# Kernel optimization log

Measured on AMD Instinct MI355X. Metric: run time of the kernel, lower is better.

## Reference

```python
import jax, jax.numpy as jnp
import numpy as np

TAU = 0.25
N_TIMESTEPS = 12


def setup_inputs() -> dict:
    key = jax.random.key(0)
    ks = jax.random.split(key, 6)
    B, O, H, P, C = 2048, 512, 1024, 1024, 512
    sc = lambda k, shape: jax.random.normal(k, shape, dtype=jnp.float32) * (1.0 / np.sqrt(shape[0]))
    return {
        "inputs": jax.random.normal(ks[0], (B, O), dtype=jnp.float32),
        "w_oh": sc(ks[1], (O, H)),
        "w_hp": sc(ks[2], (H, P)),
        "w_pp": sc(ks[3], (P, P)),
        "w_pc": sc(ks[4], (P, C)),
        "w_cp": sc(ks[5], (C, P)),
        "bias_h": jnp.zeros((H,), dtype=jnp.float32),
        "bias_p": jnp.zeros((P,), dtype=jnp.float32),
        "bias_c": jnp.zeros((C,), dtype=jnp.float32),
    }


def reference(inputs, w_oh, w_hp, w_pp, w_pc, w_cp, bias_h, bias_p, bias_c):
    tau = jnp.float32(TAU)
    one_m_tau = jnp.float32(1.0 - TAU)
    act = jax.nn.sigmoid
    B = inputs.shape[0]
    H, P, C = w_oh.shape[1], w_pp.shape[0], w_pc.shape[1]

    # tf.linalg.set_diag(w_pp, zeros) -> zero the self-connections
    w_pp0 = w_pp * (1.0 - jnp.eye(P, dtype=w_pp.dtype))
    # orth->hidden input is constant across timesteps
    oh = inputs @ w_oh + bias_h  # [B, H]

    h0 = jnp.zeros((B, H), dtype=inputs.dtype)
    p0 = jnp.zeros((B, P), dtype=inputs.dtype)
    c0 = jnp.zeros((B, C), dtype=inputs.dtype)
    ah0 = jnp.full((B, H), 0.5, dtype=inputs.dtype)
    ap0 = jnp.full((B, P), 0.5, dtype=inputs.dtype)
    ac0 = jnp.full((B, C), 0.5, dtype=inputs.dtype)

    def step(carry, _):
        h, p, c, ah, ap, ac = carry  # states and activations from t-1
        h_n = tau * oh + one_m_tau * h
        ah_n = act(h_n)
        # p update uses t-1 activations (per original indexing)
        p_n = tau * (ah @ w_hp + ap @ w_pp0 + ac @ w_cp + bias_p) + one_m_tau * p
        ap_n = act(p_n)
        c_n = tau * (ap @ w_pc + bias_c) + one_m_tau * c
        ac_n = act(c_n)
        return (h_n, p_n, c_n, ah_n, ap_n, ac_n), ap_n

    _, act_p_seq = jax.lax.scan(step, (h0, p0, c0, ah0, ap0, ac0), None, length=N_TIMESTEPS)
    return act_p_seq  # [T, B, P] = act_p_list[1:]
```

## Files before the change

### kernel.cpp

```cpp
#include <hip/hip_runtime.h>
#include <stdint.h>
#include <math.h>

typedef __attribute__((ext_vector_type(8))) short short8;
typedef __attribute__((ext_vector_type(4))) float floatx4;

#define B_DIM 2048
#define O_DIM 512
#define H_DIM 1024
#define P_DIM 1024
#define C_DIM 512
#define K_BIG 2560
#define TAU 0.25f
#define OMT 0.75f

#define VMCNT(n) (((n) & 15) | (((n) >> 4) << 14) | 0x0F70)
#define MEMFENCE asm volatile("" ::: "memory")

__device__ inline short f2bf(float f) {
  uint32_t u = __float_as_uint(f);
  u += 0x7FFFu + ((u >> 16) & 1u);
  return (short)(u >> 16);
}

__device__ inline float sigmoidf_(float x) {
  return 1.0f / (1.0f + __expf(-x));
}

__device__ inline void async_copy16(const void* g, void* l) {
  __builtin_amdgcn_global_load_lds((__attribute__((address_space(1))) void*)g,
                                   (__attribute__((address_space(3))) void*)l,
                                   16, 0, 0);
}

__device__ inline void gemm_core64(const short* __restrict__ A, int lda,
                                   const short* __restrict__ BT, int ldb,
                                   int Ktot, short* lds, floatx4 acc[2][2]) {
  const int tid = threadIdx.x, lane = tid & 63, w = tid >> 6;
  const int wm = w >> 1, wn = w & 1;
  const int fm = lane & 15, hi = lane >> 4;

  const int r0 = tid >> 3;
  const int g0 = (tid & 7) ^ (r0 & 7);
  const short* gA0 = A + (size_t)r0 * lda + g0 * 8;
  const short* gA1 = A + (size_t)(r0 + 32) * lda + g0 * 8;
  const short* gB0 = BT + (size_t)r0 * ldb + g0 * 8;
  const short* gB1 = BT + (size_t)(r0 + 32) * ldb + g0 * 8;
  const int dA0 = tid * 8, dA1 = (256 + tid) * 8;
  const int dB0 = 4096 + tid * 8, dB1 = 4096 + (256 + tid) * 8;

  const int nIter = Ktot >> 6;

  auto stage = [&](int t) {
    short* d = lds + (t % 3) * 8192;
    int ko = t * 64;
    async_copy16(gA0 + ko, d + dA0);
    async_copy16(gA1 + ko, d + dA1);
    async_copy16(gB0 + ko, d + dB0);
    async_copy16(gB1 + ko, d + dB1);
  };

  const int sw = fm & 7;

  stage(0);
  stage(1);
  for (int it = 0; it < nIter; ++it) {
    if (it + 1 < nIter) __builtin_amdgcn_s_waitcnt(VMCNT(4));
    else                __builtin_amdgcn_s_waitcnt(VMCNT(0));
    MEMFENCE;
    __builtin_amdgcn_s_barrier();
    MEMFENCE;
    if (it + 2 < nIter) stage(it + 2);
    const short* sb = lds + (it % 3) * 8192;
#pragma unroll
    for (int sl = 0; sl < 2; ++sl) {
      short8 a[2], b[2];
#pragma unroll
      for (int i = 0; i < 2; ++i) {
        int ar = wm * 32 + i * 16 + fm;
        a[i] = *(const short8*)&sb[(ar * 8 + ((sl * 4 + hi) ^ sw)) * 8];
      }
#pragma unroll
      for (int j = 0; j < 2; ++j) {
        int br = wn * 32 + j * 16 + fm;
        b[j] = *(const short8*)&sb[4096 + (br * 8 + ((sl * 4 + hi) ^ sw)) * 8];
      }
#pragma unroll
      for (int i = 0; i < 2; ++i)
#pragma unroll
        for (int j = 0; j < 2; ++j)
          acc[i][j] = __builtin_amdgcn_mfma_f32_16x16x32_bf16(a[i], b[j], acc[i][j], 0, 0, 0);
    }
  }
  MEMFENCE;
}

__device__ inline void gemm_core128(const short* __restrict__ A, int lda,
                                    const short* __restrict__ BT, int ldb,
                                    int Ktot, short* lds, floatx4 acc[4][2]) {
  const int tid = threadIdx.x, lane = tid & 63, w = tid >> 6;
  const int wm = w >> 1, wn = w & 1;
  const int fm = lane & 15, hi = lane >> 4;

  const int r0 = tid >> 3;
  const int g0 = (tid & 7) ^ (r0 & 7);
  const short* gA0 = A + (size_t)r0 * lda + g0 * 8;
  const short* gA1 = A + (size_t)(r0 + 32) * lda + g0 * 8;
  const short* gA2 = A + (size_t)(r0 + 64) * lda + g0 * 8;
  const short* gA3 = A + (size_t)(r0 + 96) * lda + g0 * 8;
  const short* gB0 = BT + (size_t)r0 * ldb + g0 * 8;
  const short* gB1 = BT + (size_t)(r0 + 32) * ldb + g0 * 8;
  const int dA0 = tid * 8,          dA1 = (256 + tid) * 8;
  const int dA2 = (512 + tid) * 8,  dA3 = (768 + tid) * 8;
  const int dB0 = 8192 + tid * 8,   dB1 = 8192 + (256 + tid) * 8;

  const int nIter = Ktot >> 6;

  auto stage = [&](int t) {
    short* d = lds + (t % 3) * 12288;
    int ko = t * 64;
    async_copy16(gA0 + ko, d + dA0);
    async_copy16(gA1 + ko, d + dA1);
    async_copy16(gA2 + ko, d + dA2);
    async_copy16(gA3 + ko, d + dA3);
    async_copy16(gB0 + ko, d + dB0);
    async_copy16(gB1 + ko, d + dB1);
  };

  const int sw = fm & 7;

  stage(0);
  stage(1);
  for (int it = 0; it < nIter; ++it) {
    if (it + 1 < nIter) __builtin_amdgcn_s_waitcnt(VMCNT(6));
    else                __builtin_amdgcn_s_waitcnt(VMCNT(0));
    MEMFENCE;
    __builtin_amdgcn_s_barrier();
    MEMFENCE;
    if (it + 2 < nIter) stage(it + 2);
    const short* sb = lds + (it % 3) * 12288;
#pragma unroll
    for (int sl = 0; sl < 2; ++sl) {
      short8 a[4], b[2];
#pragma unroll
      for (int i = 0; i < 4; ++i) {
        int ar = wm * 64 + i * 16 + fm;
        a[i] = *(const short8*)&sb[(ar * 8 + ((sl * 4 + hi) ^ sw)) * 8];
      }
#pragma unroll
      for (int j = 0; j < 2; ++j) {
        int br = wn * 32 + j * 16 + fm;
        b[j] = *(const short8*)&sb[8192 + (br * 8 + ((sl * 4 + hi) ^ sw)) * 8];
      }
#pragma unroll
      for (int i = 0; i < 4; ++i)
#pragma unroll
        for (int j = 0; j < 2; ++j)
          acc[i][j] = __builtin_amdgcn_mfma_f32_16x16x32_bf16(a[i], b[j], acc[i][j], 0, 0, 0);
    }
  }
  MEMFENCE;
}


__global__ void k_build_wb(const float* __restrict__ w_hp, const float* __restrict__ w_pp,
                           const float* __restrict__ w_cp, short* __restrict__ WbT) {
  int idx = blockIdx.x * 256 + threadIdx.x;
  int n = idx / K_BIG, k = idx - n * K_BIG;
  float v;
  if (k < 1024) v = w_hp[k * P_DIM + n];
  else if (k < 2048) { int r = k - 1024; v = (r == n) ? 0.f : w_pp[r * P_DIM + n]; }
  else v = w_cp[(k - 2048) * P_DIM + n];
  WbT[idx] = f2bf(v);
}

__global__ void k_build_pc(const float* __restrict__ w_pc, short* __restrict__ WpcT) {
  int idx = blockIdx.x * 256 + threadIdx.x;
  int n = idx >> 10, k = idx & 1023;
  WpcT[idx] = f2bf(w_pc[k * C_DIM + n]);
}

__global__ void k_build_woh(const float* __restrict__ w_oh, short* __restrict__ WohT) {
  int idx = blockIdx.x * 256 + threadIdx.x;
  int n = idx >> 9, k = idx & 511;
  WohT[idx] = f2bf(w_oh[k * H_DIM + n]);
}

__global__ void k_build_in(const float* __restrict__ inp, short* __restrict__ inb) {
  int idx = blockIdx.x * 256 + threadIdx.x;
  inb[idx] = f2bf(inp[idx]);
}

__global__ void k_init(uint32_t* __restrict__ X0, float* __restrict__ p, float* __restrict__ c) {
  int i = blockIdx.x * 256 + threadIdx.x;
  X0[i] = 0x3F003F00u;
  if (i < B_DIM * P_DIM) p[i] = 0.f;
  if (i < B_DIM * C_DIM) c[i] = 0.f;
}

__global__ __launch_bounds__(256, 2) void k_gemm_oh(const short* __restrict__ inb,
                                                    const short* __restrict__ WohT,
                                                    const float* __restrict__ bias_h,
                                                    float* __restrict__ oh) {
  __shared__ short lds[36864];
  floatx4 acc[4][2] = {};
  int m0 = (blockIdx.x & 15) * 128, n0 = (blockIdx.x >> 4) * 64;
  gemm_core128(inb + (size_t)m0 * O_DIM, O_DIM, WohT + (size_t)n0 * O_DIM, O_DIM,
               O_DIM, lds, acc);
  const int lane = threadIdx.x & 63;
  const int fm = lane & 15, hi = lane >> 4;
  const int w = threadIdx.x >> 6, wm = w >> 1, wn = w & 1;
#pragma unroll
  for (int i = 0; i < 4; ++i)
#pragma unroll
    for (int j = 0; j < 2; ++j)
#pragma unroll
      for (int r = 0; r < 4; ++r) {
        int m = m0 + wm * 64 + i * 16 + hi * 4 + r;
        int n = n0 + wn * 32 + j * 16 + fm;
        oh[(size_t)m * H_DIM + n] = acc[i][j][r] + bias_h[n];
      }
}

__global__ __launch_bounds__(256, 2) void k_step(const short* __restrict__ Xc,
                                                 short* __restrict__ Xn,
                                                 const short* __restrict__ WbT,
                                                 const short* __restrict__ WpcT,
                                                 const float* __restrict__ bias_p,
                                                 const float* __restrict__ bias_c,
                                                 const float* __restrict__ oh,
                                                 float* __restrict__ p,
                                                 float* __restrict__ c,
                                                 float* __restrict__ out_t,
                                                 float ct) {
  __shared__ short lds[36864];
  const int lane = threadIdx.x & 63;
  const int fm = lane & 15, hi = lane >> 4;
  const int w = threadIdx.x >> 6, wm = w >> 1, wn = w & 1;
  const int bx = blockIdx.x;

  if (bx < 256) {
    floatx4 acc[4][2] = {};
    int m0 = (bx & 15) * 128, n0 = (bx >> 4) * 64;
    gemm_core128(Xc + (size_t)m0 * K_BIG, K_BIG, WbT + (size_t)n0 * K_BIG, K_BIG,
                 K_BIG, lds, acc);
#pragma unroll
    for (int i = 0; i < 4; ++i)
#pragma unroll
      for (int j = 0; j < 2; ++j)
#pragma unroll
        for (int r = 0; r < 4; ++r) {
          int m = m0 + wm * 64 + i * 16 + hi * 4 + r;
          int n = n0 + wn * 32 + j * 16 + fm;
          size_t o = (size_t)m * P_DIM + n;
          float pn = TAU * (acc[i][j][r] + bias_p[n]) + OMT * p[o];
          p[o] = pn;
          float ap = sigmoidf_(pn);
          out_t[o] = ap;
          Xn[(size_t)m * K_BIG + H_DIM + n] = f2bf(ap);
          float ah = sigmoidf_(ct * oh[o]);
          Xn[(size_t)m * K_BIG + n] = f2bf(ah);
        }
  } else {
    floatx4 acc[2][2] = {};
    int v = bx - 256;
    int m0 = (v >> 3) * 64, n0 = (v & 7) * 64;
    gemm_core64(Xc + (size_t)m0 * K_BIG + H_DIM, K_BIG, WpcT + (size_t)n0 * P_DIM,
                P_DIM, P_DIM, lds, acc);
#pragma unroll
    for (int i = 0; i < 2; ++i)
#pragma unroll
      for (int j = 0; j < 2; ++j)
#pragma unroll
        for (int r = 0; r < 4; ++r) {
          int m = m0 + wm * 32 + i * 16 + hi * 4 + r;
          int n = n0 + wn * 32 + j * 16 + fm;
          size_t o = (size_t)m * C_DIM + n;
          float cn = TAU * (acc[i][j][r] + bias_c[n]) + OMT * c[o];
          c[o] = cn;
          Xn[(size_t)m * K_BIG + H_DIM + P_DIM + n] = f2bf(sigmoidf_(cn));
        }
  }
}

extern "C" void kernel_launch(void* const* d_in, const int* in_sizes, int n_in,
                              void* d_out, int out_size, void* d_ws, size_t ws_size,
                              hipStream_t stream) {
  const float* inputs = (const float*)d_in[0];
  const float* w_oh   = (const float*)d_in[1];
  const float* w_hp   = (const float*)d_in[2];
  const float* w_pp   = (const float*)d_in[3];
  const float* w_pc   = (const float*)d_in[4];
  const float* w_cp   = (const float*)d_in[5];
  const float* bias_h = (const float*)d_in[6];
  const float* bias_p = (const float*)d_in[7];
  const float* bias_c = (const float*)d_in[8];
  float* out = (float*)d_out;

  char* ws = (char*)d_ws;
  auto alloc = [&](size_t bytes) {
    char* q = ws;
    ws += (bytes + 255) & ~(size_t)255;
    return q;
  };
  short* WbT  = (short*)alloc((size_t)P_DIM * K_BIG * 2);
  short* WpcT = (short*)alloc((size_t)C_DIM * P_DIM * 2);
  short* WohT = (short*)alloc((size_t)H_DIM * O_DIM * 2);
  short* inb  = (short*)alloc((size_t)B_DIM * O_DIM * 2);
  float* oh   = (float*)alloc((size_t)B_DIM * H_DIM * 4);
  short* X0   = (short*)alloc((size_t)B_DIM * K_BIG * 2);
  short* X1   = (short*)alloc((size_t)B_DIM * K_BIG * 2);
  float* p    = (float*)alloc((size_t)B_DIM * P_DIM * 4);
  float* c    = (float*)alloc((size_t)B_DIM * C_DIM * 4);

  k_init<<<dim3((B_DIM * K_BIG / 2) / 256), 256, 0, stream>>>((uint32_t*)X0, p, c);
  k_build_wb<<<dim3((P_DIM * K_BIG) / 256), 256, 0, stream>>>(w_hp, w_pp, w_cp, WbT);
  k_build_pc<<<dim3((C_DIM * P_DIM) / 256), 256, 0, stream>>>(w_pc, WpcT);
  k_build_woh<<<dim3((H_DIM * O_DIM) / 256), 256, 0, stream>>>(w_oh, WohT);
  k_build_in<<<dim3((B_DIM * O_DIM) / 256), 256, 0, stream>>>(inputs, inb);
  k_gemm_oh<<<dim3(256), 256, 0, stream>>>(inb, WohT, bias_h, oh);

  short* Xbuf[2] = {X0, X1};
  for (int t = 1; t <= 12; ++t) {
    float ct = 1.0f - powf(OMT, (float)t);
    k_step<<<dim3(512), 256, 0, stream>>>(Xbuf[(t + 1) & 1], Xbuf[t & 1],
                                          WbT, WpcT, bias_p, bias_c, oh, p, c,
                                          out + (size_t)(t - 1) * B_DIM * P_DIM, ct);
  }
}
```

Measured before the change: 510.4 us.

## Precompute hidden-activation GEMM for all steps and shrink recurrent K

After: 484.6 us. 1.05x faster.

```diff
diff --git a/kernel.cpp b/kernel.cpp
--- a/kernel.cpp
+++ b/kernel.cpp
@@ -11,6 +11,7 @@
 #define P_DIM 1024
 #define C_DIM 512
 #define K_BIG 2560
+#define K_REC 1536
 #define TAU 0.25f
 #define OMT 0.75f
 
@@ -162,6 +163,66 @@
   MEMFENCE;
 }
 
+__device__ inline void gemm_core128sq(const short* __restrict__ A, int lda,
+                                      const short* __restrict__ BT, int ldb,
+                                      int Ktot, short* lds, floatx4 acc[4][4]) {
+  const int tid = threadIdx.x, lane = tid & 63, w = tid >> 6;
+  const int wm = w >> 1, wn = w & 1;
+  const int fm = lane & 15, hi = lane >> 4;
+
+  const int r0 = tid >> 2;
+  const int c0 = tid & 3;
+  const int g0 = c0 ^ (r0 & 3);
+  const short* gA0 = A + (size_t)r0 * lda + g0 * 8;
+  const short* gA1 = A + (size_t)(r0 + 64) * lda + g0 * 8;
+  const short* gB0 = BT + (size_t)r0 * ldb + g0 * 8;
+  const short* gB1 = BT + (size_t)(r0 + 64) * ldb + g0 * 8;
+  const int dA0 = tid * 8, dA1 = (256 + tid) * 8;
+  const int dB0 = 4096 + tid * 8, dB1 = 4096 + (256 + tid) * 8;
+
+  const int nIter = Ktot >> 5;
+
+  auto stage = [&](int t) {
+    short* d = lds + (t % 3) * 8192;
+    int ko = t * 32;
+    async_copy16(gA0 + ko, d + dA0);
+    async_copy16(gA1 + ko, d + dA1);
+    async_copy16(gB0 + ko, d + dB0);
+    async_copy16(gB1 + ko, d + dB1);
+  };
+
+  const int swz = fm & 3;
+
+  stage(0);
+  stage(1);
+  for (int it = 0; it < nIter; ++it) {
+    if (it + 1 < nIter) __builtin_amdgcn_s_waitcnt(VMCNT(4));
+    else                __builtin_amdgcn_s_waitcnt(VMCNT(0));
+    MEMFENCE;
+    __builtin_amdgcn_s_barrier();
+    MEMFENCE;
+    if (it + 2 < nIter) stage(it + 2);
+    const short* sb = lds + (it % 3) * 8192;
+    short8 a[4], b[4];
+#pragma unroll
+    for (int i = 0; i < 4; ++i) {
+      int ar = wm * 64 + i * 16 + fm;
+      a[i] = *(const short8*)&sb[(ar * 4 + (hi ^ swz)) * 8];
+    }
+#pragma unroll
+    for (int j = 0; j < 4; ++j) {
+      int br = wn * 64 + j * 16 + fm;
+      b[j] = *(const short8*)&sb[4096 + (br * 4 + (hi ^ swz)) * 8];
+    }
+#pragma unroll
+    for (int i = 0; i < 4; ++i)
+#pragma unroll
+      for (int j = 0; j < 4; ++j)
+        acc[i][j] = __builtin_amdgcn_mfma_f32_16x16x32_bf16(a[i], b[j], acc[i][j], 0, 0, 0);
+  }
+  MEMFENCE;
+}
+
 
 __global__ void k_build_wb(const float* __restrict__ w_hp, const float* __restrict__ w_pp,
                            const float* __restrict__ w_cp, short* __restrict__ WbT) {
@@ -189,13 +250,6 @@
 __global__ void k_build_in(const float* __restrict__ inp, short* __restrict__ inb) {
   int idx = blockIdx.x * 256 + threadIdx.x;
   inb[idx] = f2bf(inp[idx]);
-}
-
-__global__ void k_init(uint32_t* __restrict__ X0, float* __restrict__ p, float* __restrict__ c) {
-  int i = blockIdx.x * 256 + threadIdx.x;
-  X0[i] = 0x3F003F00u;
-  if (i < B_DIM * P_DIM) p[i] = 0.f;
-  if (i < B_DIM * C_DIM) c[i] = 0.f;
 }
 
 __global__ __launch_bounds__(256, 2) void k_gemm_oh(const short* __restrict__ inb,
@@ -222,51 +276,136 @@
       }
 }
 
-__global__ __launch_bounds__(256, 2) void k_step(const short* __restrict__ Xc,
+__global__ void k_ah(const float* __restrict__ oh, short* __restrict__ Ah) {
+  int tp = blockIdx.y + 1;
+  float o = 1.0f;
+  for (int i = 0; i < 11; ++i) if (i < tp) o *= OMT;
+  float ct = 1.0f - o;
+  size_t idx = ((size_t)blockIdx.x * 256 + threadIdx.x) * 8;
+  const float4* s = (const float4*)(oh + idx);
+  float4 v0 = s[0], v1 = s[1];
+  short8 r;
+  r[0] = f2bf(sigmoidf_(ct * v0.x)); r[1] = f2bf(sigmoidf_(ct * v0.y));
+  r[2] = f2bf(sigmoidf_(ct * v0.z)); r[3] = f2bf(sigmoidf_(ct * v0.w));
+  r[4] = f2bf(sigmoidf_(ct * v1.x)); r[5] = f2bf(sigmoidf_(ct * v1.y));
+  r[6] = f2bf(sigmoidf_(ct * v1.z)); r[7] = f2bf(sigmoidf_(ct * v1.w));
+  *(short8*)(Ah + (size_t)blockIdx.y * B_DIM * H_DIM + idx) = r;
+}
+
+__global__ __launch_bounds__(256, 3) void k_pah(const short* __restrict__ Ah,
+                                                const short* __restrict__ WbT,
+                                                float* __restrict__ Pdst) {
+  __shared__ short lds[24576];
+  floatx4 acc[4][4] = {};
+  int m = blockIdx.x % 176, n = blockIdx.x / 176;
+  int m0 = m * 128, n0 = n * 128;
+  gemm_core128sq(Ah + (size_t)m0 * H_DIM, H_DIM, WbT + (size_t)n0 * K_BIG, K_BIG,
+                 H_DIM, lds, acc);
+  const int lane = threadIdx.x & 63;
+  const int fm = lane & 15, hi = lane >> 4;
+  const int w = threadIdx.x >> 6, wm = w >> 1, wn = w & 1;
+#pragma unroll
+  for (int i = 0; i < 4; ++i)
+#pragma unroll
+    for (int j = 0; j < 4; ++j)
+#pragma unroll
+      for (int r = 0; r < 4; ++r) {
+        int rr = m0 + wm * 64 + i * 16 + hi * 4 + r;
+        int nn = n0 + wn * 64 + j * 16 + fm;
+        Pdst[(size_t)rr * P_DIM + nn] = acc[i][j][r];
+      }
+}
+
+__global__ void k_step1a(const short* __restrict__ WbT, const short* __restrict__ WpcT,
+                         const float* __restrict__ bias_p, const float* __restrict__ bias_c,
+                         float* __restrict__ p1v, float* __restrict__ ap1v,
+                         float* __restrict__ c1v, float* __restrict__ ac1v) {
+  int r = blockIdx.x * 4 + (threadIdx.x >> 6);
+  int lane = threadIdx.x & 63;
+  float s = 0.f;
+  if (r < 1024) {
+    const short* row = WbT + (size_t)r * K_BIG;
+    for (int k = lane; k < K_BIG; k += 64)
+      s += __uint_as_float(((uint32_t)(uint16_t)row[k]) << 16);
+  } else {
+    const short* row = WpcT + (size_t)(r - 1024) * P_DIM;
+    for (int k = lane; k < P_DIM; k += 64)
+      s += __uint_as_float(((uint32_t)(uint16_t)row[k]) << 16);
+  }
+#pragma unroll
+  for (int off = 32; off > 0; off >>= 1) s += __shfl_down(s, off, 64);
+  if (lane == 0) {
+    if (r < 1024) {
+      float pv = TAU * (0.5f * s + bias_p[r]);
+      p1v[r] = pv; ap1v[r] = sigmoidf_(pv);
+    } else {
+      int n = r - 1024;
+      float cv = TAU * (0.5f * s + bias_c[n]);
+      c1v[n] = cv; ac1v[n] = sigmoidf_(cv);
+    }
+  }
+}
+
+__global__ void k_step1b(const float* __restrict__ p1v, const float* __restrict__ ap1v,
+                         const float* __restrict__ c1v, const float* __restrict__ ac1v,
+                         short* __restrict__ X1, float* __restrict__ p,
+                         float* __restrict__ c, float* __restrict__ out0) {
+  int n = blockIdx.x * 256 + threadIdx.x;
+  int m = blockIdx.y;
+  if (n < 1024) {
+    float ap = ap1v[n];
+    X1[(size_t)m * K_REC + n] = f2bf(ap);
+    out0[(size_t)m * P_DIM + n] = ap;
+    p[(size_t)m * P_DIM + n] = p1v[n];
+  } else {
+    int nn = n - 1024;
+    X1[(size_t)m * K_REC + n] = f2bf(ac1v[nn]);
+    c[(size_t)m * C_DIM + nn] = c1v[nn];
+  }
+}
+
+__global__ __launch_bounds__(256, 3) void k_step(const short* __restrict__ Xc,
                                                  short* __restrict__ Xn,
                                                  const short* __restrict__ WbT,
                                                  const short* __restrict__ WpcT,
                                                  const float* __restrict__ bias_p,
                                                  const float* __restrict__ bias_c,
-                                                 const float* __restrict__ oh,
                                                  float* __restrict__ p,
                                                  float* __restrict__ c,
-                                                 float* __restrict__ out_t,
-                                                 float ct) {
-  __shared__ short lds[36864];
+                                                 float* __restrict__ out_t) {
+  __shared__ short lds[24576];
+  floatx4 acc[2][2] = {};
   const int lane = threadIdx.x & 63;
   const int fm = lane & 15, hi = lane >> 4;
   const int w = threadIdx.x >> 6, wm = w >> 1, wn = w & 1;
   const int bx = blockIdx.x;
 
-  if (bx < 256) {
-    floatx4 acc[4][2] = {};
-    int m0 = (bx & 15) * 128, n0 = (bx >> 4) * 64;
-    gemm_core128(Xc + (size_t)m0 * K_BIG, K_BIG, WbT + (size_t)n0 * K_BIG, K_BIG,
-                 K_BIG, lds, acc);
-#pragma unroll
-    for (int i = 0; i < 4; ++i)
+  if (bx < 512) {
+    int m0 = (bx & 31) * 64, n0 = (bx >> 5) * 64;
+    gemm_core64(Xc + (size_t)m0 * K_REC, K_REC,
+                WbT + (size_t)n0 * K_BIG + H_DIM, K_BIG,
+                K_REC, lds, acc);
+#pragma unroll
+    for (int i = 0; i < 2; ++i)
 #pragma unroll
       for (int j = 0; j < 2; ++j)
 #pragma unroll
         for (int r = 0; r < 4; ++r) {
-          int m = m0 + wm * 64 + i * 16 + hi * 4 + r;
+          int m = m0 + wm * 32 + i * 16 + hi * 4 + r;
           int n = n0 + wn * 32 + j * 16 + fm;
           size_t o = (size_t)m * P_DIM + n;
-          float pn = TAU * (acc[i][j][r] + bias_p[n]) + OMT * p[o];
+          float pn = TAU * (acc[i][j][r] + out_t[o] + bias_p[n]) + OMT * p[o];
           p[o] = pn;
           float ap = sigmoidf_(pn);
           out_t[o] = ap;
-          Xn[(size_t)m * K_BIG + H_DIM + n] = f2bf(ap);
-          float ah = sigmoidf_(ct * oh[o]);
-          Xn[(size_t)m * K_BIG + n] = f2bf(ah);
+          Xn[(size_t)m * K_REC + n] = f2bf(ap);
         }
   } else {
-    floatx4 acc[2][2] = {};
-    int v = bx - 256;
+    int v = bx - 512;
     int m0 = (v >> 3) * 64, n0 = (v & 7) * 64;
-    gemm_core64(Xc + (size_t)m0 * K_BIG + H_DIM, K_BIG, WpcT + (size_t)n0 * P_DIM,
-                P_DIM, P_DIM, lds, acc);
+    gemm_core64(Xc + (size_t)m0 * K_REC, K_REC,
+                WpcT + (size_t)n0 * P_DIM, P_DIM,
+                P_DIM, lds, acc);
 #pragma unroll
     for (int i = 0; i < 2; ++i)
 #pragma unroll
@@ -278,7 +417,7 @@
           size_t o = (size_t)m * C_DIM + n;
           float cn = TAU * (acc[i][j][r] + bias_c[n]) + OMT * c[o];
           c[o] = cn;
-          Xn[(size_t)m * K_BIG + H_DIM + P_DIM + n] = f2bf(sigmoidf_(cn));
+          Xn[(size_t)m * K_REC + H_DIM + n] = f2bf(sigmoidf_(cn));
         }
   }
 }
@@ -308,23 +447,33 @@
   short* WohT = (short*)alloc((size_t)H_DIM * O_DIM * 2);
   short* inb  = (short*)alloc((size_t)B_DIM * O_DIM * 2);
   float* oh   = (float*)alloc((size_t)B_DIM * H_DIM * 4);
-  short* X0   = (short*)alloc((size_t)B_DIM * K_BIG * 2);
-  short* X1   = (short*)alloc((size_t)B_DIM * K_BIG * 2);
+  short* Ah   = (short*)alloc((size_t)11 * B_DIM * H_DIM * 2);
+  short* XA   = (short*)alloc((size_t)B_DIM * K_REC * 2);
+  short* XB   = (short*)alloc((size_t)B_DIM * K_REC * 2);
   float* p    = (float*)alloc((size_t)B_DIM * P_DIM * 4);
   float* c    = (float*)alloc((size_t)B_DIM * C_DIM * 4);
-
-  k_init<<<dim3((B_DIM * K_BIG / 2) / 256), 256, 0, stream>>>((uint32_t*)X0, p, c);
+  float* p1v  = (float*)alloc(1024 * 4);
+  float* ap1v = (float*)alloc(1024 * 4);
+  float* c1v  = (float*)alloc(512 * 4);
+  float* ac1v = (float*)alloc(512 * 4);
+
   k_build_wb<<<dim3((P_DIM * K_BIG) / 256), 256, 0, stream>>>(w_hp, w_pp, w_cp, WbT);
   k_build_pc<<<dim3((C_DIM * P_DIM) / 256), 256, 0, stream>>>(w_pc, WpcT);
   k_build_woh<<<dim3((H_DIM * O_DIM) / 256), 256, 0, stream>>>(w_oh, WohT);
   k_build_in<<<dim3((B_DIM * O_DIM) / 256), 256, 0, stream>>>(inputs, inb);
+
   k_gemm_oh<<<dim3(256), 256, 0, stream>>>(inb, WohT, bias_h, oh);
-
-  short* Xbuf[2] = {X0, X1};
-  for (int t = 1; t <= 12; ++t) {
-    float ct = 1.0f - powf(OMT, (float)t);
-    k_step<<<dim3(512), 256, 0, stream>>>(Xbuf[(t + 1) & 1], Xbuf[t & 1],
-                                          WbT, WpcT, bias_p, bias_c, oh, p, c,
-                                          out + (size_t)(t - 1) * B_DIM * P_DIM, ct);
-  }
-}
+  k_ah<<<dim3((B_DIM * H_DIM) / (256 * 8), 11), 256, 0, stream>>>(oh, Ah);
+
+  k_pah<<<dim3(1408), 256, 0, stream>>>(Ah, WbT, out + (size_t)B_DIM * P_DIM);
+
+  k_step1a<<<dim3(384), 256, 0, stream>>>(WbT, WpcT, bias_p, bias_c, p1v, ap1v, c1v, ac1v);
+  k_step1b<<<dim3(6, 2048), 256, 0, stream>>>(p1v, ap1v, c1v, ac1v, XA, p, c, out);
+
+  short* Xs[2] = {XB, XA};
+  for (int t = 2; t <= 12; ++t) {
+    k_step<<<dim3(768), 256, 0, stream>>>(Xs[(t - 1) & 1], Xs[t & 1],
+                                          WbT, WpcT, bias_p, bias_c, p, c,
+                                          out + (size_t)(t - 1) * B_DIM * P_DIM);
+  }
+}
```
